# Optimization experiments

Measured on AMD Instinct MI355X. Metric: run time of the kernel, lower is better.

Reference implementation:

```python
import jax, jax.numpy as jnp
import numpy as np

N = 3072          # n_vertices
D = 512           # embedding_size (hardcoded in module)
ALPHA = 0.2       # LeakyReLU slope
AVG_DEG = 32
NEG_INF = -9e15
N_ITERS = 10
TRIPLET_MARGIN = 400.0


def setup_inputs() -> dict:
    key = jax.random.key(0)
    ks = jax.random.split(key, 14)
    s = 0.05  # weight init scale
    emb = jax.random.normal(ks[0], (N, D), dtype=jnp.float32) * 0.1
    # symmetric 0/1 adjacency, no self loops, density ~ AVG_DEG/N
    u = jax.random.uniform(ks[1], (N, N))
    A = jnp.triu((u < (AVG_DEG / N)).astype(jnp.float32), 1)
    adj = A + A.T
    rn = lambda k, shp: jax.random.normal(k, shp, dtype=jnp.float32) * s
    return {
        "embeddings": emb,
        "adj": adj,
        "W_n": rn(ks[2], (D, D)), "a_src_n": rn(ks[3], (D,)), "a_dst_n": rn(ks[4], (D,)),
        "W_nn": rn(ks[5], (D, D)), "a_src_nn": rn(ks[6], (D,)), "a_dst_nn": rn(ks[7], (D,)),
        "W_u": rn(ks[8], (2 * D, D)), "b_u": jnp.zeros((D,), dtype=jnp.float32),
        "W_g": rn(ks[9], (D, D)), "a_src_g": rn(ks[10], (D,)), "a_dst_g": rn(ks[11], (D,)),
    }


def _gat_attention(h, adj, W, a_src, a_dst):
    # standard pyGAT layer: Wh = hW; e_ij = LeakyReLU(a_src.Wh_i + a_dst.Wh_j)
    Wh = h @ W                                   # [N, D]
    e = jax.nn.leaky_relu((Wh @ a_src)[:, None] + (Wh @ a_dst)[None, :], ALPHA)
    att = jax.nn.softmax(jnp.where(adj > 0, e, NEG_INF), axis=1)  # [N, N]
    return att, Wh


def reference(embeddings, adj, W_n, a_src_n, a_dst_n, W_nn, a_src_nn, a_dst_nn,
              W_u, b_u, W_g, a_src_g, a_dst_g):
    n = embeddings.shape[0]
    inv_adj = 1.0 - adj - jnp.eye(n, dtype=adj.dtype)  # non-neighbors, no self
    emb = embeddings
    for _ in range(N_ITERS):
        att_n, Wh_n = _gat_attention(emb, adj, W_n, a_src_n, a_dst_n)
        neigh = jax.nn.elu(att_n @ Wh_n)               # concat=True -> ELU
        att_nn, Wh_nn = _gat_attention(emb, inv_adj, W_nn, a_src_nn, a_dst_nn)
        non_neigh = jax.nn.elu(att_nn @ Wh_nn)
        cat = jnp.concatenate([neigh, non_neigh], axis=1)  # [N, 2D]
        emb = jax.nn.relu(emb + cat @ W_u + b_u)
    sq = jnp.sum(emb * emb, axis=1)
    d2 = sq[:, None] + sq[None, :] - 2.0 * (emb @ emb.T)
    dist = jnp.sqrt(jnp.maximum(d2, 1e-12))            # [N, N]
    embedding_loss = jnp.sum(dist * (-adj))
    triplet_loss = jnp.maximum(embedding_loss + TRIPLET_MARGIN, 0.0)
    # glimpse layer returns the attention matrix itself
    att_g, _ = _gat_attention(emb, adj, W_g, a_src_g, a_dst_g)
    confidence = jnp.max(att_g, axis=1)
    log_conf = jnp.mean(jnp.log(confidence + 1e-8) - jnp.log(1e-8))
    return jnp.stack([triplet_loss, embedding_loss, log_conf])
```

## Files before the change

### kernel.cpp

```cpp
#include <hip/hip_runtime.h>
#include <math.h>

#define N_V 3072
#define D_E 512
#define EDGE_CAP 128
constexpr float LRELU_ALPHA = 0.2f;
constexpr float NEG_INF_F = -9e15f;

typedef __attribute__((ext_vector_type(8))) short bf16x8;
typedef __attribute__((ext_vector_type(4))) float f32x4;
typedef __attribute__((ext_vector_type(4))) unsigned short ushort4v;
typedef __attribute__((ext_vector_type(2))) unsigned short ushort2v;

__device__ inline unsigned short f2bf(float f) {
    union { float f; unsigned int u; } x; x.f = f;
    unsigned int r = x.u + 0x7fffu + ((x.u >> 16) & 1u);
    return (unsigned short)(r >> 16);
}
__device__ inline float bf2f(unsigned short b) {
    union { unsigned int u; float f; } x; x.u = ((unsigned int)b) << 16;
    return x.f;
}

__device__ inline void xcd_swizzle(int& bx, int& by) {
    int gx = gridDim.x, nwg = gx * gridDim.y;
    int flat = by * gx + bx;
    int q = nwg >> 3;
    int swz = (flat & 7) * q + (flat >> 3);
    bx = swz % gx; by = swz / gx;
}

template<int EPI>
__global__ __launch_bounds__(256) void gemm_bf16(
    const unsigned short* __restrict__ A,
    const unsigned short* __restrict__ BT,
    int M, int N, int K,
    unsigned short* __restrict__ C0, int ldc0,
    unsigned short* __restrict__ C1,
    const float* __restrict__ addv,
    const float* __restrict__ bias,
    float* __restrict__ Cf)
{
    constexpr int BM = 128, BN = 64, BK = 64;
    __shared__ unsigned short As[BM * BK];
    __shared__ unsigned short Bs[BN * BK];
    const int tid  = threadIdx.x;
    int bxi = blockIdx.x, byi = blockIdx.y;
    xcd_swizzle(bxi, byi);
    const int bm   = byi * BM, bn = bxi * BN;
    const int lane = tid & 63, wid = tid >> 6;
    const int wr   = wid >> 1, wc = wid & 1;
    const int lr   = lane & 15, lk = lane >> 4;

    f32x4 acc[4][2];
    #pragma unroll
    for (int i = 0; i < 4; ++i)
        #pragma unroll
        for (int j = 0; j < 2; ++j)
            acc[i][j] = (f32x4)(0.f);

    auto asp = (__attribute__((address_space(3))) unsigned short*)As;
    auto bsp = (__attribute__((address_space(3))) unsigned short*)Bs;

    for (int k0 = 0; k0 < K; k0 += BK) {
        #pragma unroll
        for (int l = 0; l < 4; ++l) {
            int li = l * 256 + tid;
            int row = li >> 3, slot = li & 7;
            int gs = slot ^ (row & 7);
            __builtin_amdgcn_global_load_lds(
                (const __attribute__((address_space(1))) void*)(A + (size_t)(bm + row) * K + k0 + gs * 8),
                (__attribute__((address_space(3))) void*)(asp + li * 8), 16, 0, 0);
        }
        #pragma unroll
        for (int l = 0; l < 2; ++l) {
            int li = l * 256 + tid;
            int row = li >> 3, slot = li & 7;
            int gs = slot ^ (row & 7);
            __builtin_amdgcn_global_load_lds(
                (const __attribute__((address_space(1))) void*)(BT + (size_t)(bn + row) * K + k0 + gs * 8),
                (__attribute__((address_space(3))) void*)(bsp + li * 8), 16, 0, 0);
        }
        __syncthreads();

        #pragma unroll
        for (int ks = 0; ks < 2; ++ks) {
            bf16x8 af[4], bfr[2];
            #pragma unroll
            for (int fm = 0; fm < 4; ++fm) {
                int row = wr * 64 + fm * 16 + lr;
                int sl = (ks * 4 + lk) ^ (row & 7);
                af[fm] = *(const bf16x8*)(As + row * BK + sl * 8);
            }
            #pragma unroll
            for (int fn = 0; fn < 2; ++fn) {
                int col = wc * 32 + fn * 16 + lr;
                int sl = (ks * 4 + lk) ^ (col & 7);
                bfr[fn] = *(const bf16x8*)(Bs + col * BK + sl * 8);
            }
            #pragma unroll
            for (int fm = 0; fm < 4; ++fm)
                #pragma unroll
                for (int fn = 0; fn < 2; ++fn)
                    acc[fm][fn] = __builtin_amdgcn_mfma_f32_16x16x32_bf16(
                        af[fm], bfr[fn], acc[fm][fn], 0, 0, 0);
        }
        __syncthreads();
    }

    #pragma unroll
    for (int fm = 0; fm < 4; ++fm) {
        #pragma unroll
        for (int fn = 0; fn < 2; ++fn) {
            int row0 = bm + wr * 64 + fm * 16 + lk * 4;
            int col  = bn + wc * 32 + fn * 16 + lr;
            f32x4 v = acc[fm][fn];
            if (EPI == 2) {
                #pragma unroll
                for (int r = 0; r < 4; ++r) {
                    float x = v[r] + addv[(size_t)(row0 + r) * N + col] + bias[col];
                    x = x > 0.f ? x : 0.f;
                    Cf[(size_t)(row0 + r) * N + col] = x;
                    C0[(size_t)(row0 + r) * ldc0 + col] = f2bf(x);
                }
            } else {
                if (col < 512) {
                    #pragma unroll
                    for (int r = 0; r < 4; ++r)
                        C0[(size_t)(row0 + r) * ldc0 + col] = f2bf(v[r]);
                } else {
                    ushort4v p;
                    p.x = f2bf(v[0]); p.y = f2bf(v[1]);
                    p.z = f2bf(v[2]); p.w = f2bf(v[3]);
                    *(ushort4v*)(C1 + (size_t)(col - 512) * M + row0) = p;
                }
            }
        }
    }
}

template<int SPLITK>
__global__ __launch_bounds__(256) void gemm_bf16_sk(
    const unsigned short* __restrict__ A,
    const unsigned short* __restrict__ BT,
    int M, int N, int K,
    float* __restrict__ Cp)
{
    constexpr int BM = 128, BN = 128, BK = 64;
    __shared__ unsigned short As[BM * BK];
    __shared__ unsigned short Bs[BN * BK];
    const int tid  = threadIdx.x;
    int bxi = blockIdx.x, byi = blockIdx.y;
    xcd_swizzle(bxi, byi);
    const int bm   = byi * BM, bn = bxi * BN;
    const int kh   = K / SPLITK;
    const int kbeg = blockIdx.z * kh, kend = kbeg + kh;
    const int lane = tid & 63, wid = tid >> 6;
    const int wr   = wid >> 1, wc = wid & 1;
    const int lr   = lane & 15, lk = lane >> 4;

    f32x4 acc[4][4];
    #pragma unroll
    for (int i = 0; i < 4; ++i)
        #pragma unroll
        for (int j = 0; j < 4; ++j)
            acc[i][j] = (f32x4)(0.f);

    auto asp = (__attribute__((address_space(3))) unsigned short*)As;
    auto bsp = (__attribute__((address_space(3))) unsigned short*)Bs;

    for (int k0 = kbeg; k0 < kend; k0 += BK) {
        #pragma unroll
        for (int l = 0; l < 4; ++l) {
            int li = l * 256 + tid;
            int row = li >> 3, slot = li & 7;
            int gs = slot ^ (row & 7);
            __builtin_amdgcn_global_load_lds(
                (const __attribute__((address_space(1))) void*)(A + (size_t)(bm + row) * K + k0 + gs * 8),
                (__attribute__((address_space(3))) void*)(asp + li * 8), 16, 0, 0);
        }
        #pragma unroll
        for (int l = 0; l < 4; ++l) {
            int li = l * 256 + tid;
            int row = li >> 3, slot = li & 7;
            int gs = slot ^ (row & 7);
            __builtin_amdgcn_global_load_lds(
                (const __attribute__((address_space(1))) void*)(BT + (size_t)(bn + row) * K + k0 + gs * 8),
                (__attribute__((address_space(3))) void*)(bsp + li * 8), 16, 0, 0);
        }
        __syncthreads();

        #pragma unroll
        for (int ks = 0; ks < 2; ++ks) {
            bf16x8 af[4], bfr[4];
            #pragma unroll
            for (int fm = 0; fm < 4; ++fm) {
                int row = wr * 64 + fm * 16 + lr;
                int sl = (ks * 4 + lk) ^ (row & 7);
                af[fm] = *(const bf16x8*)(As + row * BK + sl * 8);
            }
            #pragma unroll
            for (int fn = 0; fn < 4; ++fn) {
                int col = wc * 64 + fn * 16 + lr;
                int sl = (ks * 4 + lk) ^ (col & 7);
                bfr[fn] = *(const bf16x8*)(Bs + col * BK + sl * 8);
            }
            #pragma unroll
            for (int fm = 0; fm < 4; ++fm)
                #pragma unroll
                for (int fn = 0; fn < 4; ++fn)
                    acc[fm][fn] = __builtin_amdgcn_mfma_f32_16x16x32_bf16(
                        af[fm], bfr[fn], acc[fm][fn], 0, 0, 0);
        }
        __syncthreads();
    }

    float* Cz = Cp + (size_t)blockIdx.z * M * N;
    #pragma unroll
    for (int fm = 0; fm < 4; ++fm) {
        #pragma unroll
        for (int fn = 0; fn < 4; ++fn) {
            int row0 = bm + wr * 64 + fm * 16 + lk * 4;
            int col  = bn + wc * 64 + fn * 16 + lr;
            #pragma unroll
            for (int r = 0; r < 4; ++r)
                Cz[(size_t)(row0 + r) * N + col] = acc[fm][fn][r];
        }
    }
}

__global__ __launch_bounds__(256) void elu_combine4(
    const float* __restrict__ Cp, unsigned short* __restrict__ cat)
{
    int idx = blockIdx.x * 256 + threadIdx.x;
    const size_t S = (size_t)N_V * D_E;
    float4 a = ((const float4*)Cp)[idx];
    float4 b = ((const float4*)(Cp + S))[idx];
    float4 c = ((const float4*)(Cp + 2 * S))[idx];
    float4 d = ((const float4*)(Cp + 3 * S))[idx];
    int r = idx >> 7;
    int cc = (idx & 127) * 4;
    float v[4] = { a.x + b.x + c.x + d.x, a.y + b.y + c.y + d.y,
                   a.z + b.z + c.z + d.z, a.w + b.w + c.w + d.w };
    ushort4v o;
    #pragma unroll
    for (int q = 0; q < 4; ++q) {
        float x = v[q];
        x = x > 0.f ? x : (expf(x) - 1.f);
        ((unsigned short*)&o)[q] = f2bf(x);
    }
    *(ushort4v*)(cat + (size_t)r * (2 * D_E) + D_E + cc) = o;
}

__global__ __launch_bounds__(256) void convT_f32_bf16(
    const float* __restrict__ W, unsigned short* __restrict__ WT, int K, int Nw)
{
    int k = blockIdx.x * 256 + threadIdx.x;
    int n = blockIdx.y;
    if (k < K) WT[(size_t)n * K + k] = f2bf(W[(size_t)k * Nw + n]);
}

__global__ __launch_bounds__(256) void conv_bf16(
    const float* __restrict__ X, unsigned short* __restrict__ Y, int n)
{
    int i = blockIdx.x * 256 + threadIdx.x;
    if (i < n) Y[i] = f2bf(X[i]);
}

__global__ __launch_bounds__(256) void build_graph(
    const float* __restrict__ adj, int* __restrict__ edges,
    int* __restrict__ deg, unsigned int* __restrict__ bitmask)
{
    const int i = blockIdx.x, t = threadIdx.x;
    __shared__ int cnts[256];
    unsigned int word = 0;
    int c = 0;
    if (t < 96) {
        #pragma unroll
        for (int b = 0; b < 32; ++b) {
            int j = t * 32 + b;
            if (adj[(size_t)i * N_V + j] > 0.f) { word |= (1u << b); ++c; }
        }
    }
    cnts[t] = c;
    __syncthreads();
    for (int o = 1; o < 256; o <<= 1) {
        int add = (t >= o) ? cnts[t - o] : 0;
        __syncthreads();
        cnts[t] += add;
        __syncthreads();
    }
    int base = cnts[t] - c;
    if (t < 96) {
        int k = 0;
        #pragma unroll
        for (int b = 0; b < 32; ++b) {
            if ((word >> b) & 1u) {
                int pos = base + k;
                if (pos < EDGE_CAP) edges[(size_t)i * EDGE_CAP + pos] = t * 32 + b;
                ++k;
            }
        }
        bitmask[(size_t)i * 96 + t] = word;
    }
    if (t == 0) deg[i] = cnts[255] < EDGE_CAP ? cnts[255] : EDGE_CAP;
}

__global__ __launch_bounds__(256) void matvec6(
    const float* __restrict__ W_n, const float* __restrict__ W_nn,
    const float* __restrict__ W_g,
    const float* __restrict__ as_n, const float* __restrict__ ad_n,
    const float* __restrict__ as_nn, const float* __restrict__ ad_nn,
    const float* __restrict__ as_g, const float* __restrict__ ad_g,
    float* __restrict__ wv)
{
    const int wave = threadIdx.x >> 6, lane = threadIdx.x & 63;
    const int r = blockIdx.x * 4 + wave;
    float a0 = 0, a1 = 0, a2 = 0, a3 = 0, a4 = 0, a5 = 0;
    #pragma unroll
    for (int k = 0; k < 8; ++k) {
        int c = lane + k * 64;
        float wn = W_n[(size_t)r * D_E + c];
        float wm = W_nn[(size_t)r * D_E + c];
        float wg = W_g[(size_t)r * D_E + c];
        a0 = fmaf(wn, as_n[c], a0);  a1 = fmaf(wn, ad_n[c], a1);
        a2 = fmaf(wm, as_nn[c], a2); a3 = fmaf(wm, ad_nn[c], a3);
        a4 = fmaf(wg, as_g[c], a4);  a5 = fmaf(wg, ad_g[c], a5);
    }
    #pragma unroll
    for (int off = 32; off; off >>= 1) {
        a0 += __shfl_down(a0, off); a1 += __shfl_down(a1, off);
        a2 += __shfl_down(a2, off); a3 += __shfl_down(a3, off);
        a4 += __shfl_down(a4, off); a5 += __shfl_down(a5, off);
    }
    if (lane == 0) {
        wv[0 * D_E + r] = a0; wv[1 * D_E + r] = a1;
        wv[2 * D_E + r] = a2; wv[3 * D_E + r] = a3;
        wv[4 * D_E + r] = a4; wv[5 * D_E + r] = a5;
    }
}

template<int NV>
__global__ __launch_bounds__(256) void sd_dots(
    const unsigned short* __restrict__ emb, const float* __restrict__ wv,
    float* __restrict__ outs)
{
    const int wave = threadIdx.x >> 6, lane = threadIdx.x & 63;
    const int i = blockIdx.x * 4 + wave;
    float acc[NV];
    #pragma unroll
    for (int v = 0; v < NV; ++v) acc[v] = 0.f;
    #pragma unroll
    for (int k = 0; k < 8; ++k) {
        int c = lane + k * 64;
        float x = bf2f(emb[(size_t)i * D_E + c]);
        #pragma unroll
        for (int v = 0; v < NV; ++v) acc[v] = fmaf(x, wv[v * D_E + c], acc[v]);
    }
    #pragma unroll
    for (int off = 32; off; off >>= 1)
        #pragma unroll
        for (int v = 0; v < NV; ++v) acc[v] += __shfl_down(acc[v], off);
    if (lane == 0)
        #pragma unroll
        for (int v = 0; v < NV; ++v) outs[v * N_V + i] = acc[v];
}

__global__ __launch_bounds__(256) void nn_sm_gather(
    const unsigned int* __restrict__ bitmask,
    const int* __restrict__ edges, const int* __restrict__ deg,
    const float* __restrict__ sd,
    const unsigned short* __restrict__ Whn,
    unsigned short* __restrict__ att, unsigned short* __restrict__ cat)
{
    const int t = threadIdx.x;
    __shared__ float red[256];
    if (blockIdx.x < N_V) {
        const int i = blockIdx.x;
        const float* s = sd + 2 * N_V;
        const float* dvec = sd + 3 * N_V;
        __shared__ unsigned int mrow[96];
        if (t < 96) mrow[t] = bitmask[(size_t)i * 96 + t];
        __syncthreads();
        const float si = s[i];
        const float4* dv4 = (const float4*)dvec;
        float e[3][4];
        float mloc = -3.4e38f;
        #pragma unroll
        for (int l = 0; l < 3; ++l) {
            int jv = t + l * 256;
            float4 d = dv4[jv];
            int j0 = jv * 4;
            unsigned int w = mrow[j0 >> 5];
            #pragma unroll
            for (int c = 0; c < 4; ++c) {
                int j = j0 + c;
                bool keep = (((w >> (j & 31)) & 1u) == 0u) && (j != i);
                float x = si + ((const float*)&d)[c];
                x = x > 0.f ? x : LRELU_ALPHA * x;
                e[l][c] = keep ? x : NEG_INF_F;
                mloc = fmaxf(mloc, e[l][c]);
            }
        }
        red[t] = mloc; __syncthreads();
        for (int o = 128; o; o >>= 1) {
            if (t < o) red[t] = fmaxf(red[t], red[t + o]);
            __syncthreads();
        }
        float m = red[0]; __syncthreads();
        float zloc = 0.f;
        #pragma unroll
        for (int l = 0; l < 3; ++l)
            #pragma unroll
            for (int c = 0; c < 4; ++c) { e[l][c] = expf(e[l][c] - m); zloc += e[l][c]; }
        red[t] = zloc; __syncthreads();
        for (int o = 128; o; o >>= 1) {
            if (t < o) red[t] += red[t + o];
            __syncthreads();
        }
        const float zinv = 1.f / red[0];
        #pragma unroll
        for (int l = 0; l < 3; ++l) {
            int jv = t + l * 256;
            ushort4v p;
            p.x = f2bf(e[l][0] * zinv); p.y = f2bf(e[l][1] * zinv);
            p.z = f2bf(e[l][2] * zinv); p.w = f2bf(e[l][3] * zinv);
            *(ushort4v*)(att + (size_t)i * N_V + (size_t)jv * 4) = p;
        }
    } else {
        const int i = blockIdx.x - N_V;
        const float* s = sd;
        const float* dvec = sd + N_V;
        const int cnt = deg[i];
        __shared__ float p[EDGE_CAP];
        __shared__ int lst[EDGE_CAP];
        float ev = -3.4e38f;
        if (t < cnt) {
            int j = edges[(size_t)i * EDGE_CAP + t];
            lst[t] = j;
            float x = s[i] + dvec[j];
            x = x > 0.f ? x : LRELU_ALPHA * x;
            p[t] = x;
            ev = x;
        }
        red[t] = ev; __syncthreads();
        for (int o = 128; o; o >>= 1) {
            if (t < o) red[t] = fmaxf(red[t], red[t + o]);
            __syncthreads();
        }
        float m = red[0]; __syncthreads();
        float pe = 0.f;
        if (t < cnt) { pe = expf(p[t] - m); p[t] = pe; }
        red[t] = pe; __syncthreads();
        for (int o = 128; o; o >>= 1) {
            if (t < o) red[t] += red[t + o];
            __syncthreads();
        }
        const float zinv = 1.f / red[0];
        float a0 = 0.f, a1 = 0.f;
        for (int e = 0; e < cnt; ++e) {
            int j = lst[e];
            float w = p[e] * zinv;
            ushort2v h = *(const ushort2v*)(Whn + (size_t)j * D_E + t * 2);
            a0 = fmaf(w, bf2f(h.x), a0);
            a1 = fmaf(w, bf2f(h.y), a1);
        }
        a0 = a0 > 0.f ? a0 : (expf(a0) - 1.f);
        a1 = a1 > 0.f ? a1 : (expf(a1) - 1.f);
        ushort2v o2; o2.x = f2bf(a0); o2.y = f2bf(a1);
        *(ushort2v*)(cat + (size_t)i * (2 * D_E) + t * 2) = o2;
    }
}

__global__ __launch_bounds__(256) void colsum(
    const float* __restrict__ emb, float* __restrict__ musum)
{
    const int b = blockIdx.x, t = threadIdx.x;
    float s0 = 0.f, s1 = 0.f;
    for (int r = 0; r < 64; ++r) {
        const float* row = emb + (size_t)(b * 64 + r) * D_E;
        s0 += row[t];
        s1 += row[t + 256];
    }
    atomicAdd(&musum[t], s0);
    atomicAdd(&musum[t + 256], s1);
}

__global__ __launch_bounds__(256) void center_bf16(
    const float* __restrict__ emb, const float* __restrict__ musum,
    unsigned short* __restrict__ embc)
{
    int i = blockIdx.x * 256 + threadIdx.x;
    int c = i & (D_E - 1);
    embc[i] = f2bf(emb[i] - musum[c] * (1.f / N_V));
}

__global__ __launch_bounds__(256) void edge_loss_c(
    const int* __restrict__ edges, const int* __restrict__ deg,
    const unsigned short* __restrict__ embc, float* __restrict__ accum)
{
    __shared__ unsigned short rowi[D_E];
    __shared__ float gsum[16];
    const int i = blockIdx.x, t = threadIdx.x;
    if (t < 64) ((bf16x8*)rowi)[t] = ((const bf16x8*)(embc + (size_t)i * D_E))[t];
    __syncthreads();
    const int g = t >> 4, l = t & 15;
    const int cnt = deg[i];
    float sum = 0.f;
    for (int e = g; e < cnt; e += 16) {
        int j = edges[(size_t)i * EDGE_CAP + e];
        float d2 = 0.f;
        #pragma unroll
        for (int q = 0; q < 4; ++q) {
            int off = q * 128 + l * 8;
            bf16x8 a = *(const bf16x8*)(rowi + off);
            bf16x8 b = *(const bf16x8*)(embc + (size_t)j * D_E + off);
            #pragma unroll
            for (int k = 0; k < 8; ++k) {
                float df = bf2f(((unsigned short*)&a)[k]) -
                           bf2f(((unsigned short*)&b)[k]);
                d2 = fmaf(df, df, d2);
            }
        }
        #pragma unroll
        for (int msk = 1; msk < 16; msk <<= 1) d2 += __shfl_xor(d2, msk);
        if (l == 0) sum += sqrtf(fmaxf(d2, 1e-12f));
    }
    if (l == 0) gsum[g] = sum;
    __syncthreads();
    if (t == 0) {
        float tot = 0.f;
        #pragma unroll
        for (int k = 0; k < 16; ++k) tot += gsum[k];
        atomicAdd(accum, -tot);
    }
}

__global__ __launch_bounds__(256) void conf_kernel(
    const unsigned int* __restrict__ bitmask, const float* __restrict__ s,
    const float* __restrict__ dvec, float* __restrict__ accum)
{
    const int i = blockIdx.x, t = threadIdx.x;
    __shared__ unsigned int mrow[96];
    __shared__ float red[256];
    if (t < 96) mrow[t] = bitmask[(size_t)i * 96 + t];
    __syncthreads();
    const float si = s[i];
    const float4* dv4 = (const float4*)dvec;
    float e[3][4];
    float mloc = -3.4e38f;
    #pragma unroll
    for (int l = 0; l < 3; ++l) {
        int jv = t + l * 256;
        float4 d = dv4[jv];
        int j0 = jv * 4;
        unsigned int w = mrow[j0 >> 5];
        #pragma unroll
        for (int c = 0; c < 4; ++c) {
            int j = j0 + c;
            bool keep = ((w >> (j & 31)) & 1u) != 0u;
            float x = si + ((const float*)&d)[c];
            x = x > 0.f ? x : LRELU_ALPHA * x;
            e[l][c] = keep ? x : NEG_INF_F;
            mloc = fmaxf(mloc, e[l][c]);
        }
    }
    red[t] = mloc; __syncthreads();
    for (int o = 128; o; o >>= 1) {
        if (t < o) red[t] = fmaxf(red[t], red[t + o]);
        __syncthreads();
    }
    float m = red[0]; __syncthreads();
    float zloc = 0.f;
    #pragma unroll
    for (int l = 0; l < 3; ++l)
        #pragma unroll
        for (int c = 0; c < 4; ++c) zloc += expf(e[l][c] - m);
    red[t] = zloc; __syncthreads();
    for (int o = 128; o; o >>= 1) {
        if (t < o) red[t] += red[t + o];
        __syncthreads();
    }
    if (t == 0) atomicAdd(accum, logf(1.f / red[0] + 1e-8f));
}

__global__ void finalize(const float* __restrict__ accum, float* __restrict__ out)
{
    float loss = accum[0];
    out[0] = fmaxf(loss + 400.f, 0.f);
    out[1] = loss;
    out[2] = accum[1] / (float)N_V - logf(1e-8f);
}

extern "C" void kernel_launch(void* const* d_in, const int* in_sizes, int n_in,
                              void* d_out, int out_size, void* d_ws, size_t ws_size,
                              hipStream_t stream) {
    const float* emb_in   = (const float*)d_in[0];
    const float* adj      = (const float*)d_in[1];
    const float* W_n      = (const float*)d_in[2];
    const float* a_src_n  = (const float*)d_in[3];
    const float* a_dst_n  = (const float*)d_in[4];
    const float* W_nn     = (const float*)d_in[5];
    const float* a_src_nn = (const float*)d_in[6];
    const float* a_dst_nn = (const float*)d_in[7];
    const float* W_u      = (const float*)d_in[8];
    const float* b_u      = (const float*)d_in[9];
    const float* W_g      = (const float*)d_in[10];
    const float* a_src_g  = (const float*)d_in[11];
    const float* a_dst_g  = (const float*)d_in[12];
    float* out = (float*)d_out;

    char* p = (char*)d_ws;
    auto alloc = [&](size_t bytes) { char* r = p; p += (bytes + 255) & ~(size_t)255; return r; };

    unsigned short* att_nn  = (unsigned short*)alloc((size_t)N_V * N_V * 2);
    float*          Cp      = (float*)alloc((size_t)4 * N_V * D_E * 4);
    unsigned short* Whn     = (unsigned short*)alloc((size_t)N_V * D_E * 2);
    unsigned short* WhTnn   = (unsigned short*)alloc((size_t)D_E * N_V * 2);
    unsigned short* cat_bf  = (unsigned short*)alloc((size_t)N_V * 2 * D_E * 2);
    float*          embf[2] = { (float*)alloc((size_t)N_V * D_E * 4),
                                (float*)alloc((size_t)N_V * D_E * 4) };
    unsigned short* embb[2] = { (unsigned short*)alloc((size_t)N_V * D_E * 2),
                                (unsigned short*)alloc((size_t)N_V * D_E * 2) };
    unsigned short* embc    = (unsigned short*)alloc((size_t)N_V * D_E * 2);
    unsigned short* W2T     = (unsigned short*)alloc((size_t)(2 * D_E) * D_E * 2);
    unsigned short* WuT     = (unsigned short*)alloc((size_t)D_E * (2 * D_E) * 2);
    float*          wv      = (float*)alloc(6 * D_E * 4);
    float*          sd      = (float*)alloc(4 * N_V * 4);
    float*          sdg     = (float*)alloc(2 * N_V * 4);
    float*          musum   = (float*)alloc(D_E * 4);
    int*            edges   = (int*)alloc((size_t)N_V * EDGE_CAP * 4);
    int*            deg     = (int*)alloc(N_V * 4);
    unsigned int*   bitmask = (unsigned int*)alloc((size_t)N_V * 96 * 4);
    float*          accum   = (float*)alloc(2 * 4);

    dim3 blk(256);

    convT_f32_bf16<<<dim3(2, D_E), blk, 0, stream>>>(W_n, W2T, D_E, D_E);
    convT_f32_bf16<<<dim3(2, D_E), blk, 0, stream>>>(W_nn, W2T + (size_t)D_E * D_E, D_E, D_E);
    convT_f32_bf16<<<dim3(4, D_E), blk, 0, stream>>>(W_u, WuT, 2 * D_E, D_E);
    conv_bf16<<<(N_V * D_E) / 256, blk, 0, stream>>>(emb_in, embb[0], N_V * D_E);
    hipMemcpyAsync(embf[0], emb_in, (size_t)N_V * D_E * 4, hipMemcpyDeviceToDevice, stream);
    hipMemsetAsync(accum, 0, 2 * sizeof(float), stream);
    hipMemsetAsync(musum, 0, D_E * sizeof(float), stream);
    build_graph<<<N_V, blk, 0, stream>>>(adj, edges, deg, bitmask);
    matvec6<<<D_E / 4, blk, 0, stream>>>(W_n, W_nn, W_g, a_src_n, a_dst_n,
                                         a_src_nn, a_dst_nn, a_src_g, a_dst_g, wv);

    dim3 gW2(16, N_V / 128);
    dim3 gG(8, N_V / 128);
    dim3 gSK(4, N_V / 128, 4);

    int cur = 0;
    for (int it = 0; it < 10; ++it) {
        int nxt = cur ^ 1;
        sd_dots<4><<<N_V / 4, blk, 0, stream>>>(embb[cur], wv, sd);
        gemm_bf16<4><<<gW2, blk, 0, stream>>>(embb[cur], W2T, N_V, 2 * D_E, D_E,
                                              Whn, D_E, WhTnn, nullptr, nullptr, nullptr);
        nn_sm_gather<<<2 * N_V, blk, 0, stream>>>(bitmask, edges, deg, sd,
                                                  Whn, att_nn, cat_bf);
        gemm_bf16_sk<4><<<gSK, blk, 0, stream>>>(att_nn, WhTnn, N_V, D_E, N_V, Cp);
        elu_combine4<<<(N_V * D_E) / (4 * 256), blk, 0, stream>>>(Cp, cat_bf);
        gemm_bf16<2><<<gG, blk, 0, stream>>>(cat_bf, WuT, N_V, D_E, 2 * D_E,
                                             embb[nxt], D_E, nullptr, embf[cur], b_u, embf[nxt]);
        cur = nxt;
    }

    colsum<<<N_V / 64, blk, 0, stream>>>(embf[cur], musum);
    center_bf16<<<(N_V * D_E) / 256, blk, 0, stream>>>(embf[cur], musum, embc);
    edge_loss_c<<<N_V, blk, 0, stream>>>(edges, deg, embc, accum);
    sd_dots<2><<<N_V / 4, blk, 0, stream>>>(embb[cur], wv + 4 * D_E, sdg);
    conf_kernel<<<N_V, blk, 0, stream>>>(bitmask, sdg, sdg + N_V, accum + 1);

    finalize<<<1, 1, 0, stream>>>(accum, out);
}
```

Measured before the change: 912.1 us.

## Replace split-K non-neighbor GEMM with 64x64-tile GEMM fusing ELU epilogue

The split-K 128x128 GEMM, which wrote four fp32 partial buffers that a separate kernel summed and passed through ELU, is replaced by a full-K 64x64-tile GEMM. The new kernel applies ELU and writes bf16 directly into the concat buffer. This removes the partial-sum round trip through global memory and one kernel launch per iteration. In exchange, each block runs the full K=3072 loop with smaller tiles, which means less reuse per tile and scalar strided stores. Separately, the final loss reductions drop float atomics in favour of per-row partial arrays reduced by a single-block finalize kernel, which also removes a memset.

Measured after the change: 884.6 us. 3.0% less time.

```diff
diff --git a/kernel.cpp b/kernel.cpp
--- a/kernel.cpp
+++ b/kernel.cpp
@@ -139,39 +139,35 @@
     }
 }
 
-template<int SPLITK>
-__global__ __launch_bounds__(256) void gemm_bf16_sk(
+__global__ __launch_bounds__(256) void gemm_nn64(
     const unsigned short* __restrict__ A,
     const unsigned short* __restrict__ BT,
-    int M, int N, int K,
-    float* __restrict__ Cp)
-{
-    constexpr int BM = 128, BN = 128, BK = 64;
+    unsigned short* __restrict__ cat)
+{
+    constexpr int BM = 64, BN = 64, BK = 64, K = N_V;
     __shared__ unsigned short As[BM * BK];
     __shared__ unsigned short Bs[BN * BK];
-    const int tid  = threadIdx.x;
+    const int tid = threadIdx.x;
     int bxi = blockIdx.x, byi = blockIdx.y;
     xcd_swizzle(bxi, byi);
-    const int bm   = byi * BM, bn = bxi * BN;
-    const int kh   = K / SPLITK;
-    const int kbeg = blockIdx.z * kh, kend = kbeg + kh;
+    const int bm = byi * BM, bn = bxi * BN;
     const int lane = tid & 63, wid = tid >> 6;
-    const int wr   = wid >> 1, wc = wid & 1;
-    const int lr   = lane & 15, lk = lane >> 4;
-
-    f32x4 acc[4][4];
-    #pragma unroll
-    for (int i = 0; i < 4; ++i)
-        #pragma unroll
-        for (int j = 0; j < 4; ++j)
+    const int wr = wid >> 1, wc = wid & 1;
+    const int lr = lane & 15, lk = lane >> 4;
+
+    f32x4 acc[2][2];
+    #pragma unroll
+    for (int i = 0; i < 2; ++i)
+        #pragma unroll
+        for (int j = 0; j < 2; ++j)
             acc[i][j] = (f32x4)(0.f);
 
     auto asp = (__attribute__((address_space(3))) unsigned short*)As;
     auto bsp = (__attribute__((address_space(3))) unsigned short*)Bs;
 
-    for (int k0 = kbeg; k0 < kend; k0 += BK) {
-        #pragma unroll
-        for (int l = 0; l < 4; ++l) {
+    for (int k0 = 0; k0 < K; k0 += BK) {
+        #pragma unroll
+        for (int l = 0; l < 2; ++l) {
             int li = l * 256 + tid;
             int row = li >> 3, slot = li & 7;
             int gs = slot ^ (row & 7);
@@ -180,7 +176,7 @@
                 (__attribute__((address_space(3))) void*)(asp + li * 8), 16, 0, 0);
         }
         #pragma unroll
-        for (int l = 0; l < 4; ++l) {
+        for (int l = 0; l < 2; ++l) {
             int li = l * 256 + tid;
             int row = li >> 3, slot = li & 7;
             int gs = slot ^ (row & 7);
@@ -192,64 +188,43 @@
 
         #pragma unroll
         for (int ks = 0; ks < 2; ++ks) {
-            bf16x8 af[4], bfr[4];
-            #pragma unroll
-            for (int fm = 0; fm < 4; ++fm) {
-                int row = wr * 64 + fm * 16 + lr;
+            bf16x8 af[2], bfr[2];
+            #pragma unroll
+            for (int fm = 0; fm < 2; ++fm) {
+                int row = wr * 32 + fm * 16 + lr;
                 int sl = (ks * 4 + lk) ^ (row & 7);
                 af[fm] = *(const bf16x8*)(As + row * BK + sl * 8);
             }
             #pragma unroll
-            for (int fn = 0; fn < 4; ++fn) {
-                int col = wc * 64 + fn * 16 + lr;
+            for (int fn = 0; fn < 2; ++fn) {
+                int col = wc * 32 + fn * 16 + lr;
                 int sl = (ks * 4 + lk) ^ (col & 7);
                 bfr[fn] = *(const bf16x8*)(Bs + col * BK + sl * 8);
             }
             #pragma unroll
-            for (int fm = 0; fm < 4; ++fm)
+            for (int fm = 0; fm < 2; ++fm)
                 #pragma unroll
-                for (int fn = 0; fn < 4; ++fn)
+                for (int fn = 0; fn < 2; ++fn)
                     acc[fm][fn] = __builtin_amdgcn_mfma_f32_16x16x32_bf16(
                         af[fm], bfr[fn], acc[fm][fn], 0, 0, 0);
         }
         __syncthreads();
     }
 
-    float* Cz = Cp + (size_t)blockIdx.z * M * N;
-    #pragma unroll
-    for (int fm = 0; fm < 4; ++fm) {
-        #pragma unroll
-        for (int fn = 0; fn < 4; ++fn) {
-            int row0 = bm + wr * 64 + fm * 16 + lk * 4;
-            int col  = bn + wc * 64 + fn * 16 + lr;
-            #pragma unroll
-            for (int r = 0; r < 4; ++r)
-                Cz[(size_t)(row0 + r) * N + col] = acc[fm][fn][r];
-        }
-    }
-}
-
-__global__ __launch_bounds__(256) void elu_combine4(
-    const float* __restrict__ Cp, unsigned short* __restrict__ cat)
-{
-    int idx = blockIdx.x * 256 + threadIdx.x;
-    const size_t S = (size_t)N_V * D_E;
-    float4 a = ((const float4*)Cp)[idx];
-    float4 b = ((const float4*)(Cp + S))[idx];
-    float4 c = ((const float4*)(Cp + 2 * S))[idx];
-    float4 d = ((const float4*)(Cp + 3 * S))[idx];
-    int r = idx >> 7;
-    int cc = (idx & 127) * 4;
-    float v[4] = { a.x + b.x + c.x + d.x, a.y + b.y + c.y + d.y,
-                   a.z + b.z + c.z + d.z, a.w + b.w + c.w + d.w };
-    ushort4v o;
-    #pragma unroll
-    for (int q = 0; q < 4; ++q) {
-        float x = v[q];
-        x = x > 0.f ? x : (expf(x) - 1.f);
-        ((unsigned short*)&o)[q] = f2bf(x);
-    }
-    *(ushort4v*)(cat + (size_t)r * (2 * D_E) + D_E + cc) = o;
+    #pragma unroll
+    for (int fm = 0; fm < 2; ++fm) {
+        #pragma unroll
+        for (int fn = 0; fn < 2; ++fn) {
+            int row0 = bm + wr * 32 + fm * 16 + lk * 4;
+            int col  = bn + wc * 32 + fn * 16 + lr;
+            #pragma unroll
+            for (int r = 0; r < 4; ++r) {
+                float x = acc[fm][fn][r];
+                x = x > 0.f ? x : (expf(x) - 1.f);
+                cat[(size_t)(row0 + r) * (2 * D_E) + D_E + col] = f2bf(x);
+            }
+        }
+    }
 }
 
 __global__ __launch_bounds__(256) void convT_f32_bf16(
@@ -497,7 +472,7 @@
 
 __global__ __launch_bounds__(256) void edge_loss_c(
     const int* __restrict__ edges, const int* __restrict__ deg,
-    const unsigned short* __restrict__ embc, float* __restrict__ accum)
+    const unsigned short* __restrict__ embc, float* __restrict__ epart)
 {
     __shared__ unsigned short rowi[D_E];
     __shared__ float gsum[16];
@@ -532,13 +507,13 @@
         float tot = 0.f;
         #pragma unroll
         for (int k = 0; k < 16; ++k) tot += gsum[k];
-        atomicAdd(accum, -tot);
+        epart[i] = tot;
     }
 }
 
 __global__ __launch_bounds__(256) void conf_kernel(
     const unsigned int* __restrict__ bitmask, const float* __restrict__ s,
-    const float* __restrict__ dvec, float* __restrict__ accum)
+    const float* __restrict__ dvec, float* __restrict__ cpart)
 {
     const int i = blockIdx.x, t = threadIdx.x;
     __shared__ unsigned int mrow[96];
@@ -581,15 +556,33 @@
         if (t < o) red[t] += red[t + o];
         __syncthreads();
     }
-    if (t == 0) atomicAdd(accum, logf(1.f / red[0] + 1e-8f));
-}
-
-__global__ void finalize(const float* __restrict__ accum, float* __restrict__ out)
-{
-    float loss = accum[0];
-    out[0] = fmaxf(loss + 400.f, 0.f);
-    out[1] = loss;
-    out[2] = accum[1] / (float)N_V - logf(1e-8f);
+    if (t == 0) cpart[i] = logf(1.f / red[0] + 1e-8f);
+}
+
+__global__ __launch_bounds__(256) void finalize2(
+    const float* __restrict__ epart, const float* __restrict__ cpart,
+    float* __restrict__ out)
+{
+    const int t = threadIdx.x;
+    float e = 0.f, c = 0.f;
+    #pragma unroll
+    for (int k = 0; k < 12; ++k) {
+        e += epart[t + k * 256];
+        c += cpart[t + k * 256];
+    }
+    __shared__ float re[256], rc[256];
+    re[t] = e; rc[t] = c;
+    __syncthreads();
+    for (int o = 128; o; o >>= 1) {
+        if (t < o) { re[t] += re[t + o]; rc[t] += rc[t + o]; }
+        __syncthreads();
+    }
+    if (t == 0) {
+        float loss = -re[0];
+        out[0] = fmaxf(loss + 400.f, 0.f);
+        out[1] = loss;
+        out[2] = rc[0] / (float)N_V - logf(1e-8f);
+    }
 }
 
 extern "C" void kernel_launch(void* const* d_in, const int* in_sizes, int n_in,
@@ -614,7 +607,6 @@
     auto alloc = [&](size_t bytes) { char* r = p; p += (bytes + 255) & ~(size_t)255; return r; };
 
     unsigned short* att_nn  = (unsigned short*)alloc((size_t)N_V * N_V * 2);
-    float*          Cp      = (float*)alloc((size_t)4 * N_V * D_E * 4);
     unsigned short* Whn     = (unsigned short*)alloc((size_t)N_V * D_E * 2);
     unsigned short* WhTnn   = (unsigned short*)alloc((size_t)D_E * N_V * 2);
     unsigned short* cat_bf  = (unsigned short*)alloc((size_t)N_V * 2 * D_E * 2);
@@ -629,10 +621,11 @@
     float*          sd      = (float*)alloc(4 * N_V * 4);
     float*          sdg     = (float*)alloc(2 * N_V * 4);
     float*          musum   = (float*)alloc(D_E * 4);
+    float*          epart   = (float*)alloc(N_V * 4);
+    float*          cpart   = (float*)alloc(N_V * 4);
     int*            edges   = (int*)alloc((size_t)N_V * EDGE_CAP * 4);
     int*            deg     = (int*)alloc(N_V * 4);
     unsigned int*   bitmask = (unsigned int*)alloc((size_t)N_V * 96 * 4);
-    float*          accum   = (float*)alloc(2 * 4);
 
     dim3 blk(256);
 
@@ -641,7 +634,6 @@
     convT_f32_bf16<<<dim3(4, D_E), blk, 0, stream>>>(W_u, WuT, 2 * D_E, D_E);
     conv_bf16<<<(N_V * D_E) / 256, blk, 0, stream>>>(emb_in, embb[0], N_V * D_E);
     hipMemcpyAsync(embf[0], emb_in, (size_t)N_V * D_E * 4, hipMemcpyDeviceToDevice, stream);
-    hipMemsetAsync(accum, 0, 2 * sizeof(float), stream);
     hipMemsetAsync(musum, 0, D_E * sizeof(float), stream);
     build_graph<<<N_V, blk, 0, stream>>>(adj, edges, deg, bitmask);
     matvec6<<<D_E / 4, blk, 0, stream>>>(W_n, W_nn, W_g, a_src_n, a_dst_n,
@@ -649,7 +641,7 @@
 
     dim3 gW2(16, N_V / 128);
     dim3 gG(8, N_V / 128);
-    dim3 gSK(4, N_V / 128, 4);
+    dim3 gNN(D_E / 64, N_V / 64);
 
     int cur = 0;
     for (int it = 0; it < 10; ++it) {
@@ -659,8 +651,7 @@
                                               Whn, D_E, WhTnn, nullptr, nullptr, nullptr);
         nn_sm_gather<<<2 * N_V, blk, 0, stream>>>(bitmask, edges, deg, sd,
                                                   Whn, att_nn, cat_bf);
-        gemm_bf16_sk<4><<<gSK, blk, 0, stream>>>(att_nn, WhTnn, N_V, D_E, N_V, Cp);
-        elu_combine4<<<(N_V * D_E) / (4 * 256), blk, 0, stream>>>(Cp, cat_bf);
+        gemm_nn64<<<gNN, blk, 0, stream>>>(att_nn, WhTnn, cat_bf);
         gemm_bf16<2><<<gG, blk, 0, stream>>>(cat_bf, WuT, N_V, D_E, 2 * D_E,
                                              embb[nxt], D_E, nullptr, embf[cur], b_u, embf[nxt]);
         cur = nxt;
@@ -668,9 +659,9 @@
 
     colsum<<<N_V / 64, blk, 0, stream>>>(embf[cur], musum);
     center_bf16<<<(N_V * D_E) / 256, blk, 0, stream>>>(embf[cur], musum, embc);
-    edge_loss_c<<<N_V, blk, 0, stream>>>(edges, deg, embc, accum);
+    edge_loss_c<<<N_V, blk, 0, stream>>>(edges, deg, embc, epart);
     sd_dots<2><<<N_V / 4, blk, 0, stream>>>(embb[cur], wv + 4 * D_E, sdg);
-    conf_kernel<<<N_V, blk, 0, stream>>>(bitmask, sdg, sdg + N_V, accum + 1);
-
-    finalize<<<1, 1, 0, stream>>>(accum, out);
-}
+    conf_kernel<<<N_V, blk, 0, stream>>>(bitmask, sdg, sdg + N_V, cpart);
+
+    finalize2<<<1, blk, 0, stream>>>(epart, cpart, out);
+}
```
